# Optimization experiments

Hardware: AMD Instinct MI355X
Metric: run time of the kernel (lower is better)

Reference implementation:

```python
import jax, jax.numpy as jnp
import numpy as np

B, T, V, D, L, FFM = 2, 2048, 50257, 1024, 8, 2


def setup_inputs() -> dict:
    key = jax.random.key(0)
    ks = jax.random.split(key, 10)
    s = 0.02
    return {
        "input_ids": jax.random.randint(ks[0], (B, T), 0, V),
        "embed": jax.random.normal(ks[1], (V, D), jnp.float32) * s,
        "norm1_w": jnp.ones((L, D), jnp.float32),
        "norm2_w": jnp.ones((L, D), jnp.float32),
        "a_diag": jax.random.uniform(ks[2], (L, D), jnp.float32, 0.5, 0.99),
        "W_in": jax.random.normal(ks[3], (L, D, D), jnp.float32) * s,
        "b_in": jnp.zeros((L, D), jnp.float32),
        "W_out": jax.random.normal(ks[4], (L, D, D), jnp.float32) * s,
        "ff_w1": jax.random.normal(ks[5], (L, D, FFM * D), jnp.float32) * s,
        "ff_b1": jnp.zeros((L, FFM * D), jnp.float32),
        "ff_w2": jax.random.normal(ks[6], (L, FFM * D, D), jnp.float32) * s,
        "ff_b2": jnp.zeros((L, D), jnp.float32),
        "final_norm_w": jnp.ones((D,), jnp.float32),
        "lm_head_w": jax.random.normal(ks[7], (V, D), jnp.float32) * s,
    }


def rmsnorm(x, w, eps=1e-6):
    return x * jax.lax.rsqrt(jnp.mean(x * x, axis=-1, keepdims=True) + eps) * w


def chaos_core(x, a, Win, bin_, Wout):
    pre = jnp.einsum('btd,de->bte', x, Win) + bin_  # precompute input drive (parallel)

    def step(s, p):
        s = jnp.tanh(a * s + p)
        return s, s

    s0 = jnp.zeros((x.shape[0], x.shape[-1]), x.dtype)
    _, hs = jax.lax.scan(step, s0, jnp.swapaxes(pre, 0, 1))  # (T, B, D)
    hs = jnp.swapaxes(hs, 0, 1)  # (B, T, D)
    return jnp.einsum('btd,de->bte', hs, Wout)


def reference(input_ids, embed, norm1_w, norm2_w, a_diag, W_in, b_in, W_out,
              ff_w1, ff_b1, ff_w2, ff_b2, final_norm_w, lm_head_w):
    x = embed[input_ids]  # (B, T, D)
    for i in range(L):
        # input_norm -> core -> residual
        x = x + chaos_core(rmsnorm(x, norm1_w[i]), a_diag[i], W_in[i], b_in[i], W_out[i])
        # ff_norm -> FeedForward (Linear -> SiLU -> Linear) -> residual
        h = rmsnorm(x, norm2_w[i])
        h = jax.nn.silu(jnp.einsum('btd,df->btf', h, ff_w1[i]) + ff_b1[i])
        x = x + jnp.einsum('btf,fd->btd', h, ff_w2[i]) + ff_b2[i]
    x = rmsnorm(x, final_norm_w)
    return jnp.einsum('btd,vd->btv', x, lm_head_w)  # logits (B, T, V)
```

## Files before the change

### kernel.cpp

```cpp
#include <hip/hip_runtime.h>

typedef unsigned short u16;
typedef __bf16 bf16x8 __attribute__((ext_vector_type(8)));
typedef float f32x4 __attribute__((ext_vector_type(4)));
typedef unsigned short u16x4 __attribute__((ext_vector_type(4)));

__device__ __forceinline__ u16 f2bf(float f) {
  union { float f; unsigned int u; } v; v.f = f;
  return (u16)((v.u + 0x7FFFu + ((v.u >> 16) & 1u)) >> 16);
}

__device__ __forceinline__ void gload16(const void* g, void* l) {
  __builtin_amdgcn_global_load_lds(
      (const __attribute__((address_space(1))) unsigned int*)g,
      (__attribute__((address_space(3))) unsigned int*)l, 16, 0, 0);
}

__global__ void transpose_cast_kernel(const float* __restrict__ W, u16* __restrict__ WT,
                                      int R, int C) {
  __shared__ float tile[32][33];
  const int tx = threadIdx.x, ty = threadIdx.y;
  const size_t zoff = (size_t)blockIdx.z * R * C;
  const int c0 = blockIdx.x * 32, r0 = blockIdx.y * 32;
#pragma unroll
  for (int k = 0; k < 32; k += 8)
    tile[ty + k][tx] = W[zoff + (size_t)(r0 + ty + k) * C + (c0 + tx)];
  __syncthreads();
#pragma unroll
  for (int k = 0; k < 32; k += 8)
    WT[zoff + (size_t)(c0 + ty + k) * R + (r0 + tx)] = f2bf(tile[tx][ty + k]);
}

__global__ void lm_cast_kernel(const float* __restrict__ lm, u16* __restrict__ out) {
  const int row = blockIdx.x;
  const int t = threadIdx.x;
  u16x4 o = {0, 0, 0, 0};
  if (row < 50257) {
    float4 v = *(const float4*)(lm + (size_t)row * 1024 + t * 4);
    o.x = f2bf(v.x); o.y = f2bf(v.y); o.z = f2bf(v.z); o.w = f2bf(v.w);
  }
  *(u16x4*)(out + (size_t)row * 1024 + t * 4) = o;
}

__global__ void embed_kernel(const int* __restrict__ ids, const float* __restrict__ embed,
                             float* __restrict__ x) {
  const int row = blockIdx.x;
  const int id = ids[row];
  const int t = threadIdx.x;
  *(float4*)(x + (size_t)row * 1024 + t * 4) =
      *(const float4*)(embed + (size_t)id * 1024 + t * 4);
}

__global__ void norm_fused(const float* __restrict__ x, const float* __restrict__ P,
                           const float* __restrict__ bias, const float* __restrict__ w,
                           float* __restrict__ xout, u16* __restrict__ h) {
  const int row = blockIdx.x, tid = threadIdx.x;
  const size_t ro = (size_t)row * 1024 + tid * 4;
  float4 v = *(const float4*)(x + ro);
  if (P) {
    float4 a = *(const float4*)(P + ro);
    float4 b = *(const float4*)(P + 4194304 + ro);
    v.x += a.x + b.x; v.y += a.y + b.y; v.z += a.z + b.z; v.w += a.w + b.w;
  }
  if (bias) {
    float4 bb = *(const float4*)(bias + tid * 4);
    v.x += bb.x; v.y += bb.y; v.z += bb.z; v.w += bb.w;
  }
  if (xout) *(float4*)(xout + ro) = v;
  float ss = v.x * v.x + v.y * v.y + v.z * v.z + v.w * v.w;
#pragma unroll
  for (int off = 32; off; off >>= 1) ss += __shfl_xor(ss, off);
  __shared__ float red[4];
  if ((tid & 63) == 0) red[tid >> 6] = ss;
  __syncthreads();
  const float tot = red[0] + red[1] + red[2] + red[3];
  const float r = rsqrtf(tot * (1.0f / 1024.0f) + 1e-6f);
  float4 wv = *(const float4*)(w + tid * 4);
  u16x4 o;
  o.x = f2bf(v.x * r * wv.x); o.y = f2bf(v.y * r * wv.y);
  o.z = f2bf(v.z * r * wv.z); o.w = f2bf(v.w * r * wv.w);
  *(u16x4*)(h + (size_t)row * 1024 + tid * 4) = o;
}

__device__ __forceinline__ void scan_load(const float* __restrict__ p0,
                                          const float* __restrict__ p1, int tb,
                                          float A2b, float (&buf)[8]) {
#pragma unroll
  for (int j = 0; j < 8; j++)
    buf[j] = fmaf(p0[(size_t)(tb + j) * 1024] + p1[(size_t)(tb + j) * 1024],
                  2.8853900817779268f, A2b);
}

__device__ __forceinline__ void scan_comp(float (&buf)[8], float m2A2, float& r,
                                          u16* __restrict__ o, int tb) {
#pragma unroll
  for (int j = 0; j < 8; j++) {
    float z = fmaf(m2A2, r, buf[j]);
    float e = __builtin_amdgcn_exp2f(z);
    r = __builtin_amdgcn_rcpf(1.0f + e);
    o[(size_t)(tb + j) * 1024] = f2bf(fmaf(-2.0f, r, 1.0f));
  }
}

__global__ __launch_bounds__(256) void scan_kernel(const float* __restrict__ pre,
                                                   const float* __restrict__ a_diag,
                                                   const float* __restrict__ b_in,
                                                   u16* __restrict__ hs) {
  const int T = 2048;
  const int idx = blockIdx.x * 256 + threadIdx.x;
  const int b = idx >> 10, d = idx & 1023;
  const float* p0 = pre + (size_t)b * T * 1024 + d;
  const float* p1 = p0 + 4194304;
  u16* o = hs + (size_t)b * T * 1024 + d;
  const float A2 = a_diag[d] * 2.8853900817779268f;
  const float A2b = fmaf(2.8853900817779268f, b_in[d], A2);
  const float m2A2 = -2.0f * A2;
  float r = 0.5f;
  float b0[8], b1[8], b2[8], b3[8];
  scan_load(p0, p1, 0, A2b, b0); scan_load(p0, p1, 8, A2b, b1);
  scan_load(p0, p1, 16, A2b, b2); scan_load(p0, p1, 24, A2b, b3);
  for (int t0 = 0; t0 < T; t0 += 32) {
    scan_comp(b0, m2A2, r, o, t0);
    if (t0 + 32 < T) scan_load(p0, p1, t0 + 32, A2b, b0);
    scan_comp(b1, m2A2, r, o, t0 + 8);
    if (t0 + 32 < T) scan_load(p0, p1, t0 + 40, A2b, b1);
    scan_comp(b2, m2A2, r, o, t0 + 16);
    if (t0 + 32 < T) scan_load(p0, p1, t0 + 48, A2b, b2);
    scan_comp(b3, m2A2, r, o, t0 + 24);
    if (t0 + 32 < T) scan_load(p0, p1, t0 + 56, A2b, b3);
  }
}

template <int EPI>
__global__ __launch_bounds__(256) void gemm128(
    const u16* __restrict__ A, int lda, const u16* __restrict__ Bw, int ldb,
    const float* __restrict__ bias, float* Cf, u16* __restrict__ Cb, int ldc,
    int Kz, long long Cstride) {
  __shared__ char lds[65536];
  const int tid = threadIdx.x;
  const int lane = tid & 63;
  const int wid = tid >> 6;
  const int wm = wid >> 1, wn = wid & 1;
  const int tm = blockIdx.y * 128, tn = blockIdx.x * 128;
  A += (size_t)blockIdx.z * Kz;
  Bw += (size_t)blockIdx.z * Kz;
  Cf += (size_t)blockIdx.z * Cstride;

  const int srow = tid >> 3;
  const int sxor = ((tid & 7) ^ (srow & 7)) << 4;
  const char* pA = (const char*)A + (size_t)(tm + srow) * lda * 2 + sxor;
  const char* pB = (const char*)Bw + (size_t)(tn + srow) * ldb * 2 + sxor;
  const size_t pstepA = (size_t)32 * lda * 2;
  const size_t pstepB = (size_t)32 * ldb * 2;

#define STG128(kt, bufo)                                             \
  {                                                                  \
    char* d = lds + (bufo) + tid * 16;                               \
    const size_t kb = (size_t)(kt) << 7;                             \
    gload16(pA + kb, d);                                             \
    gload16(pA + pstepA + kb, d + 4096);                             \
    gload16(pA + 2 * pstepA + kb, d + 8192);                         \
    gload16(pA + 3 * pstepA + kb, d + 12288);                        \
    gload16(pB + kb, d + 16384);                                     \
    gload16(pB + pstepB + kb, d + 20480);                            \
    gload16(pB + 2 * pstepB + kb, d + 24576);                        \
    gload16(pB + 3 * pstepB + kb, d + 28672);                        \
  }

  const int lr = lane & 15;
  const int sb0 = (((lane >> 4) ^ (lane & 7)) << 4);
  const int sb[2] = {sb0, sb0 ^ 64};
  const int aB0 = (wm * 64 + lr) * 128;
  const int bB0 = 16384 + (wn * 64 + lr) * 128;

  f32x4 acc[4][4] = {};
  const int nkt = Kz >> 6;

  STG128(0, 0);
  int cur = 0;
  for (int kt = 0; kt < nkt; ++kt) {
    const bool more = (kt + 1 < nkt);
    if (more) STG128(kt + 1, (cur ^ 1) * 32768);
    if (more) { asm volatile("s_waitcnt vmcnt(8)" ::: "memory"); }
    else      { asm volatile("s_waitcnt vmcnt(0)" ::: "memory"); }
    __builtin_amdgcn_s_barrier();
    const char* base = lds + cur * 32768;
    bf16x8 aF[4][2], bF[4][2];
#pragma unroll
    for (int m = 0; m < 4; m++)
#pragma unroll
      for (int ks = 0; ks < 2; ks++) {
        aF[m][ks] = *(const bf16x8*)(base + aB0 + m * 2048 + sb[ks]);
        bF[m][ks] = *(const bf16x8*)(base + bB0 + m * 2048 + sb[ks]);
      }
#pragma unroll
    for (int ks = 0; ks < 2; ks++)
#pragma unroll
      for (int m = 0; m < 4; m++)
#pragma unroll
        for (int n = 0; n < 4; n++)
          acc[m][n] = __builtin_amdgcn_mfma_f32_16x16x32_bf16(aF[m][ks], bF[n][ks],
                                                              acc[m][n], 0, 0, 0);
    __builtin_amdgcn_s_barrier();
    cur ^= 1;
  }
#undef STG128

  const int crow = tm + wm * 64 + ((lane >> 4) << 2);
  const int ccol = tn + wn * 64 + lr;
#pragma unroll
  for (int m = 0; m < 4; m++) {
#pragma unroll
    for (int n = 0; n < 4; n++) {
      const int cg = ccol + n * 16;
      float bb = 0.0f;
      if (EPI == 2) bb = bias[cg];
#pragma unroll
      for (int j = 0; j < 4; j++) {
        const size_t off = (size_t)(crow + m * 16 + j) * ldc + cg;
        const float v = acc[m][n][j] + bb;
        if (EPI == 0) {
          Cf[off] = v;
        } else {
          const float sg = __builtin_amdgcn_rcpf(
              1.0f + __builtin_amdgcn_exp2f(-1.4426950408889634f * v));
          Cb[off] = f2bf(v * sg);
        }
      }
    }
  }
}

__global__ __launch_bounds__(512, 2) void gemm_lm8(
    const u16* __restrict__ A, const u16* __restrict__ Bw,
    float* __restrict__ C, int Nreal) {
  __shared__ char lds[131072];
  const int tid = threadIdx.x;
  const int lane = tid & 63;
  const int wid = tid >> 6;
  const int wr = wid >> 2;
  const int wc = wid & 3;
  const int bid = blockIdx.x;
  const int tm = (((bid & 7) << 1) + ((bid >> 3) & 1)) << 8;
  const int tn = (bid >> 4) << 8;

  const int srow = tid >> 3;
  const int sxor = ((tid & 7) ^ (srow & 7)) << 4;
  const char* pAs = (const char*)A + ((size_t)(tm + srow) << 11) + sxor;
  const char* pBs = (const char*)Bw + ((size_t)(tn + srow) << 11) + sxor;

#define STG(p, h, kt, ro)                                      \
  {                                                            \
    char* d = lds + (ro) + tid * 16;                           \
    const char* s = (p) + ((size_t)(h) << 18) + ((kt) << 7);   \
    gload16(s, d);                                             \
    gload16(s + (64ull << 11), d + 8192);                      \
  }

  const int lr = lane & 15;
  const int sb0 = (((lane >> 4) ^ (lane & 7)) << 4);
  const int sb[2] = {sb0, sb0 ^ 64};
  const int aB = wr * 16384 + lr * 128;
  const int bB = 32768 + (wc >> 1) * 16384 + ((wc & 1) * 64 + lr) * 128;

  bf16x8 aR[4][2], bR[2][2][2];
  f32x4 acc[8][4] = {};

#define LDA_Q(bufo, mq)                                                         \
  _Pragma("unroll") for (int m_ = 0; m_ < 4; m_++)                              \
  _Pragma("unroll") for (int k_ = 0; k_ < 2; k_++)                              \
      aR[m_][k_] = *(const bf16x8*)(lds + (bufo) + aB + (mq)*8192 + m_*2048 + sb[k_]);

#define LDB_Q(bufo, nq)                                                         \
  _Pragma("unroll") for (int n_ = 0; n_ < 2; n_++)                              \
  _Pragma("unroll") for (int k_ = 0; k_ < 2; k_++)                              \
      bR[nq][n_][k_] = *(const bf16x8*)(lds + (bufo) + bB + (nq)*4096 + n_*2048 + sb[k_]);

#define MFMA_Q(mq, nq)                                                          \
  __builtin_amdgcn_s_setprio(1);                                                \
  _Pragma("unroll") for (int m_ = 0; m_ < 4; m_++)                              \
  _Pragma("unroll") for (int n_ = 0; n_ < 2; n_++)                              \
  _Pragma("unroll") for (int k_ = 0; k_ < 2; k_++)                              \
      acc[(mq)*4 + m_][(nq)*2 + n_] = __builtin_amdgcn_mfma_f32_16x16x32_bf16(  \
          aR[m_][k_], bR[nq][n_][k_], acc[(mq)*4 + m_][(nq)*2 + n_], 0, 0, 0);  \
  __builtin_amdgcn_s_setprio(0);

#define BAR() __builtin_amdgcn_s_barrier()
#define LGKM0() asm volatile("s_waitcnt lgkmcnt(0)" ::: "memory")

  STG(pAs, 0, 0, 0);
  STG(pAs, 1, 0, 16384);
  STG(pBs, 0, 0, 32768);
  STG(pBs, 1, 0, 49152);
  STG(pBs, 0, 1, 65536 + 32768);
  STG(pBs, 1, 1, 65536 + 49152);
  asm volatile("s_waitcnt vmcnt(4)" ::: "memory");
  BAR();

  for (int it = 0; it < 8; ++it) {
    const int t1 = 2 * it + 1, t2 = 2 * it + 2, t3 = 2 * it + 3;
    const bool st = (it < 7);
    LDA_Q(0, 0); LDB_Q(0, 0);
    STG(pAs, 0, t1, 65536);
    BAR(); LGKM0(); MFMA_Q(0, 0); BAR();
    LDB_Q(0, 1);
    STG(pAs, 1, t1, 65536 + 16384);
    BAR(); LGKM0(); MFMA_Q(0, 1); BAR();
    LDA_Q(0, 1);
    if (st) STG(pBs, 0, t2, 32768);
    BAR(); LGKM0(); MFMA_Q(1, 0); BAR();
    if (st) STG(pBs, 1, t2, 49152);
    BAR(); LGKM0(); MFMA_Q(1, 1);
    if (st) { asm volatile("s_waitcnt vmcnt(4)" ::: "memory"); }
    else    { asm volatile("s_waitcnt vmcnt(0)" ::: "memory"); }
    BAR();
    LDA_Q(65536, 0); LDB_Q(65536, 0);
    if (st) STG(pAs, 0, t2, 0);
    BAR(); LGKM0(); MFMA_Q(0, 0); BAR();
    LDB_Q(65536, 1);
    if (st) STG(pAs, 1, t2, 16384);
    BAR(); LGKM0(); MFMA_Q(0, 1); BAR();
    LDA_Q(65536, 1);
    if (st) STG(pBs, 0, t3, 65536 + 32768);
    BAR(); LGKM0(); MFMA_Q(1, 0); BAR();
    if (st) STG(pBs, 1, t3, 65536 + 49152);
    BAR(); LGKM0(); MFMA_Q(1, 1);
    if (st) { asm volatile("s_waitcnt vmcnt(4)" ::: "memory"); }
    else    { asm volatile("s_waitcnt vmcnt(0)" ::: "memory"); }
    BAR();
  }
#undef STG
#undef LDA_Q
#undef LDB_Q
#undef MFMA_Q
#undef BAR
#undef LGKM0

  const int crow = tm + wr * 128 + ((lane >> 4) << 2);
  const int ccol = tn + wc * 64 + lr;
#pragma unroll
  for (int M_ = 0; M_ < 8; M_++) {
    const int r = crow + (M_ >> 2) * 64 + (M_ & 3) * 16;
#pragma unroll
    for (int N_ = 0; N_ < 4; N_++) {
      const int cg = ccol + (N_ >> 1) * 32 + (N_ & 1) * 16;
      if (cg < Nreal) {
#pragma unroll
        for (int j = 0; j < 4; j++)
          C[(size_t)(r + j) * Nreal + cg] = acc[M_][N_][j];
      }
    }
  }
}

extern "C" void kernel_launch(void* const* d_in, const int* in_sizes, int n_in,
                              void* d_out, int out_size, void* d_ws, size_t ws_size,
                              hipStream_t stream) {
  const int T = 2048, D = 1024, V = 50257, L = 8;
  const int M = 2 * T;
  const int Vpad = 50432;
  const size_t MD = (size_t)M * D;

  const int* ids = (const int*)d_in[0];
  const float* embed = (const float*)d_in[1];
  const float* norm1_w = (const float*)d_in[2];
  const float* norm2_w = (const float*)d_in[3];
  const float* a_diag = (const float*)d_in[4];
  const float* W_in = (const float*)d_in[5];
  const float* b_in = (const float*)d_in[6];
  const float* W_out = (const float*)d_in[7];
  const float* ff_w1 = (const float*)d_in[8];
  const float* ff_b1 = (const float*)d_in[9];
  const float* ff_w2 = (const float*)d_in[10];
  const float* ff_b2 = (const float*)d_in[11];
  const float* final_norm_w = (const float*)d_in[12];
  const float* lm_head_w = (const float*)d_in[13];

  char* w = (char*)d_ws;
  float* x = (float*)w;    w += MD * 4;
  u16* h = (u16*)w;        w += MD * 2;
  u16* hs = (u16*)w;       w += MD * 2;
  u16* hff = (u16*)w;      w += MD * 2 * 2;
  float* P = (float*)w;    w += MD * 4 * 2;
  float* xP = (float*)w;   w += MD * 4 * 2;
  u16* WinT = (u16*)w;     w += (size_t)L * D * D * 2;
  u16* WoutT = (u16*)w;    w += (size_t)L * D * D * 2;
  u16* ffw1T = (u16*)w;    w += (size_t)L * 2 * D * D * 2;
  u16* ffw2T = (u16*)w;    w += (size_t)L * 2 * D * D * 2;
  u16* lmpad = (u16*)w;    w += (size_t)Vpad * D * 2;

  lm_cast_kernel<<<Vpad, 256, 0, stream>>>(lm_head_w, lmpad);
  transpose_cast_kernel<<<dim3(32, 32, L), dim3(32, 8), 0, stream>>>(W_in, WinT, D, D);
  transpose_cast_kernel<<<dim3(64, 32, L), dim3(32, 8), 0, stream>>>(ff_w1, ffw1T, D, 2 * D);
  transpose_cast_kernel<<<dim3(32, 32, L), dim3(32, 8), 0, stream>>>(W_out, WoutT, D, D);
  transpose_cast_kernel<<<dim3(32, 64, L), dim3(32, 8), 0, stream>>>(ff_w2, ffw2T, 2 * D, D);

  embed_kernel<<<M, 256, 0, stream>>>(ids, embed, x);

  for (int l = 0; l < L; l++) {
    if (l == 0)
      norm_fused<<<M, 256, 0, stream>>>(x, nullptr, nullptr, norm1_w, nullptr, h);
    else
      norm_fused<<<M, 256, 0, stream>>>(x, P, ff_b2 + (size_t)(l - 1) * D,
                                        norm1_w + (size_t)l * D, x, h);
    gemm128<0><<<dim3(8, 32, 2), 256, 0, stream>>>(
        h, D, WinT + (size_t)l * D * D, D, nullptr, P, nullptr, D, 512, (long long)MD);
    scan_kernel<<<8, 256, 0, stream>>>(P, a_diag + (size_t)l * D,
                                       b_in + (size_t)l * D, hs);
    gemm128<0><<<dim3(8, 32, 2), 256, 0, stream>>>(
        hs, D, WoutT + (size_t)l * D * D, D, nullptr, xP, nullptr, D, 512, (long long)MD);
    norm_fused<<<M, 256, 0, stream>>>(x, xP, nullptr, norm2_w + (size_t)l * D, x, h);
    gemm128<2><<<dim3(16, 32, 1), 256, 0, stream>>>(
        h, D, ffw1T + (size_t)l * 2 * D * D, D, ff_b1 + (size_t)l * 2 * D,
        nullptr, hff, 2 * D, 1024, 0);
    gemm128<0><<<dim3(8, 32, 2), 256, 0, stream>>>(
        hff, 2 * D, ffw2T + (size_t)l * 2 * D * D, 2 * D, nullptr, P, nullptr, D,
        1024, (long long)MD);
  }

  norm_fused<<<M, 256, 0, stream>>>(x, P, ff_b2 + (size_t)(L - 1) * D,
                                    final_norm_w, nullptr, h);
  gemm_lm8<<<dim3(8 * 394), 512, 0, stream>>>(h, lmpad, (float*)d_out, V);
}
```

Before: 2.869 ms.

## Replace split-K GEMMs with 64x128 tiles and fuse residual adds into epilogues

Drops the split-K (z=2) 128x128 GEMMs and the partial-sum buffers. It uses a 64x128-tile GEMM over the full K, whose epilogue accumulates straight into the residual x (with bias for FF2). The norm kernels no longer read and sum two partials plus bias, and the scan reads a single pre buffer. The LM head output now uses nontemporal stores. This removes extra partial-buffer traffic and the reduction work, but it gives up K-parallelism and uses read-modify-write epilogues with smaller tiles.

Measured after the change: 3.027 ms. 1.06x slower.

```diff
diff --git a/kernel.cpp b/kernel.cpp
--- a/kernel.cpp
+++ b/kernel.cpp
@@ -51,22 +51,11 @@
       *(const float4*)(embed + (size_t)id * 1024 + t * 4);
 }
 
-__global__ void norm_fused(const float* __restrict__ x, const float* __restrict__ P,
-                           const float* __restrict__ bias, const float* __restrict__ w,
-                           float* __restrict__ xout, u16* __restrict__ h) {
+__global__ void rmsnorm_kernel(const float* __restrict__ x, const float* __restrict__ w,
+                               u16* __restrict__ out) {
   const int row = blockIdx.x, tid = threadIdx.x;
-  const size_t ro = (size_t)row * 1024 + tid * 4;
-  float4 v = *(const float4*)(x + ro);
-  if (P) {
-    float4 a = *(const float4*)(P + ro);
-    float4 b = *(const float4*)(P + 4194304 + ro);
-    v.x += a.x + b.x; v.y += a.y + b.y; v.z += a.z + b.z; v.w += a.w + b.w;
-  }
-  if (bias) {
-    float4 bb = *(const float4*)(bias + tid * 4);
-    v.x += bb.x; v.y += bb.y; v.z += bb.z; v.w += bb.w;
-  }
-  if (xout) *(float4*)(xout + ro) = v;
+  const float* xr = x + (size_t)row * 1024;
+  float4 v = *(const float4*)(xr + tid * 4);
   float ss = v.x * v.x + v.y * v.y + v.z * v.z + v.w * v.w;
 #pragma unroll
   for (int off = 32; off; off >>= 1) ss += __shfl_xor(ss, off);
@@ -79,20 +68,18 @@
   u16x4 o;
   o.x = f2bf(v.x * r * wv.x); o.y = f2bf(v.y * r * wv.y);
   o.z = f2bf(v.z * r * wv.z); o.w = f2bf(v.w * r * wv.w);
-  *(u16x4*)(h + (size_t)row * 1024 + tid * 4) = o;
-}
-
-__device__ __forceinline__ void scan_load(const float* __restrict__ p0,
-                                          const float* __restrict__ p1, int tb,
-                                          float A2b, float (&buf)[8]) {
+  *(u16x4*)(out + (size_t)row * 1024 + tid * 4) = o;
+}
+
+__device__ __forceinline__ void sload(const float* __restrict__ p, int tb,
+                                      float A2b, float (&buf)[8]) {
 #pragma unroll
   for (int j = 0; j < 8; j++)
-    buf[j] = fmaf(p0[(size_t)(tb + j) * 1024] + p1[(size_t)(tb + j) * 1024],
-                  2.8853900817779268f, A2b);
-}
-
-__device__ __forceinline__ void scan_comp(float (&buf)[8], float m2A2, float& r,
-                                          u16* __restrict__ o, int tb) {
+    buf[j] = fmaf(p[(size_t)(tb + j) * 1024], 2.8853900817779268f, A2b);
+}
+
+__device__ __forceinline__ void scomp(float (&buf)[8], float m2A2, float& r,
+                                      u16* __restrict__ o, int tb) {
 #pragma unroll
   for (int j = 0; j < 8; j++) {
     float z = fmaf(m2A2, r, buf[j]);
@@ -109,122 +96,123 @@
   const int T = 2048;
   const int idx = blockIdx.x * 256 + threadIdx.x;
   const int b = idx >> 10, d = idx & 1023;
-  const float* p0 = pre + (size_t)b * T * 1024 + d;
-  const float* p1 = p0 + 4194304;
+  const float* p = pre + (size_t)b * T * 1024 + d;
   u16* o = hs + (size_t)b * T * 1024 + d;
   const float A2 = a_diag[d] * 2.8853900817779268f;
   const float A2b = fmaf(2.8853900817779268f, b_in[d], A2);
   const float m2A2 = -2.0f * A2;
   float r = 0.5f;
   float b0[8], b1[8], b2[8], b3[8];
-  scan_load(p0, p1, 0, A2b, b0); scan_load(p0, p1, 8, A2b, b1);
-  scan_load(p0, p1, 16, A2b, b2); scan_load(p0, p1, 24, A2b, b3);
+  sload(p, 0, A2b, b0); sload(p, 8, A2b, b1);
+  sload(p, 16, A2b, b2); sload(p, 24, A2b, b3);
   for (int t0 = 0; t0 < T; t0 += 32) {
-    scan_comp(b0, m2A2, r, o, t0);
-    if (t0 + 32 < T) scan_load(p0, p1, t0 + 32, A2b, b0);
-    scan_comp(b1, m2A2, r, o, t0 + 8);
-    if (t0 + 32 < T) scan_load(p0, p1, t0 + 40, A2b, b1);
-    scan_comp(b2, m2A2, r, o, t0 + 16);
-    if (t0 + 32 < T) scan_load(p0, p1, t0 + 48, A2b, b2);
-    scan_comp(b3, m2A2, r, o, t0 + 24);
-    if (t0 + 32 < T) scan_load(p0, p1, t0 + 56, A2b, b3);
+    scomp(b0, m2A2, r, o, t0);
+    if (t0 + 32 < T) sload(p, t0 + 32, A2b, b0);
+    scomp(b1, m2A2, r, o, t0 + 8);
+    if (t0 + 32 < T) sload(p, t0 + 40, A2b, b1);
+    scomp(b2, m2A2, r, o, t0 + 16);
+    if (t0 + 32 < T) sload(p, t0 + 48, A2b, b2);
+    scomp(b3, m2A2, r, o, t0 + 24);
+    if (t0 + 32 < T) sload(p, t0 + 56, A2b, b3);
   }
 }
 
 template <int EPI>
-__global__ __launch_bounds__(256) void gemm128(
+__global__ __launch_bounds__(256) void gemmL(
     const u16* __restrict__ A, int lda, const u16* __restrict__ Bw, int ldb,
-    const float* __restrict__ bias, float* Cf, u16* __restrict__ Cb, int ldc,
-    int Kz, long long Cstride) {
-  __shared__ char lds[65536];
+    const float* __restrict__ bias, float* Cf, u16* __restrict__ Cb,
+    int ldc, int K) {
+  __shared__ char lds[49152];
   const int tid = threadIdx.x;
   const int lane = tid & 63;
-  const int wid = tid >> 6;
-  const int wm = wid >> 1, wn = wid & 1;
-  const int tm = blockIdx.y * 128, tn = blockIdx.x * 128;
-  A += (size_t)blockIdx.z * Kz;
-  Bw += (size_t)blockIdx.z * Kz;
-  Cf += (size_t)blockIdx.z * Cstride;
+  const int wc = tid >> 6;
+  const int tm = blockIdx.y * 64, tn = blockIdx.x * 128;
+  const int lr = lane & 15;
+  const int sb0 = ((lane >> 4) ^ (lane & 7)) << 4;
 
   const int srow = tid >> 3;
-  const int sxor = ((tid & 7) ^ (srow & 7)) << 4;
-  const char* pA = (const char*)A + (size_t)(tm + srow) * lda * 2 + sxor;
-  const char* pB = (const char*)Bw + (size_t)(tn + srow) * ldb * 2 + sxor;
-  const size_t pstepA = (size_t)32 * lda * 2;
-  const size_t pstepB = (size_t)32 * ldb * 2;
-
-#define STG128(kt, bufo)                                             \
-  {                                                                  \
-    char* d = lds + (bufo) + tid * 16;                               \
-    const size_t kb = (size_t)(kt) << 7;                             \
-    gload16(pA + kb, d);                                             \
-    gload16(pA + pstepA + kb, d + 4096);                             \
-    gload16(pA + 2 * pstepA + kb, d + 8192);                         \
-    gload16(pA + 3 * pstepA + kb, d + 12288);                        \
-    gload16(pB + kb, d + 16384);                                     \
-    gload16(pB + pstepB + kb, d + 20480);                            \
-    gload16(pB + 2 * pstepB + kb, d + 24576);                        \
-    gload16(pB + 3 * pstepB + kb, d + 28672);                        \
-  }
-
-  const int lr = lane & 15;
-  const int sb0 = (((lane >> 4) ^ (lane & 7)) << 4);
-  const int sb[2] = {sb0, sb0 ^ 64};
-  const int aB0 = (wm * 64 + lr) * 128;
-  const int bB0 = 16384 + (wn * 64 + lr) * 128;
-
-  f32x4 acc[4][4] = {};
-  const int nkt = Kz >> 6;
-
-  STG128(0, 0);
+  const int sxs = ((tid & 7) ^ (srow & 7)) << 4;
+  const char* pA = (const char*)A + (size_t)(tm + srow) * lda * 2 + sxs;
+  const char* pB = (const char*)Bw + (size_t)(tn + srow) * ldb * 2 + sxs;
+  const size_t a32 = (size_t)lda * 64;
+  const size_t b32 = (size_t)ldb * 64;
+
+#define STGL(kt, bufo)                                \
+  {                                                   \
+    char* d = lds + (bufo) + tid * 16;                \
+    const size_t kb = (size_t)(kt) << 7;              \
+    gload16(pA + kb, d);                              \
+    gload16(pA + a32 + kb, d + 4096);                 \
+    gload16(pB + kb, d + 8192);                       \
+    gload16(pB + b32 + kb, d + 12288);                \
+    gload16(pB + 2 * b32 + kb, d + 16384);            \
+    gload16(pB + 3 * b32 + kb, d + 20480);            \
+  }
+
+  f32x4 acc[4][2] = {};
+  const int nkt = K >> 6;
+
+  STGL(0, 0);
   int cur = 0;
   for (int kt = 0; kt < nkt; ++kt) {
-    const bool more = (kt + 1 < nkt);
-    if (more) STG128(kt + 1, (cur ^ 1) * 32768);
-    if (more) { asm volatile("s_waitcnt vmcnt(8)" ::: "memory"); }
-    else      { asm volatile("s_waitcnt vmcnt(0)" ::: "memory"); }
+    if (kt + 1 < nkt) {
+      STGL(kt + 1, (cur ^ 1) * 24576);
+      asm volatile("s_waitcnt vmcnt(6)" ::: "memory");
+    } else {
+      asm volatile("s_waitcnt vmcnt(0)" ::: "memory");
+    }
     __builtin_amdgcn_s_barrier();
-    const char* base = lds + cur * 32768;
-    bf16x8 aF[4][2], bF[4][2];
+    const char* base = lds + cur * 24576;
+    bf16x8 aF[4][2], bF[2][2];
 #pragma unroll
     for (int m = 0; m < 4; m++)
 #pragma unroll
-      for (int ks = 0; ks < 2; ks++) {
-        aF[m][ks] = *(const bf16x8*)(base + aB0 + m * 2048 + sb[ks]);
-        bF[m][ks] = *(const bf16x8*)(base + bB0 + m * 2048 + sb[ks]);
-      }
+      for (int ks = 0; ks < 2; ks++)
+        aF[m][ks] =
+            *(const bf16x8*)(base + (m * 16 + lr) * 128 + (sb0 ^ (ks << 6)));
+#pragma unroll
+    for (int n = 0; n < 2; n++)
+#pragma unroll
+      for (int ks = 0; ks < 2; ks++)
+        bF[n][ks] = *(const bf16x8*)(base + 8192 +
+                                     (wc * 32 + n * 16 + lr) * 128 +
+                                     (sb0 ^ (ks << 6)));
 #pragma unroll
     for (int ks = 0; ks < 2; ks++)
 #pragma unroll
       for (int m = 0; m < 4; m++)
 #pragma unroll
-        for (int n = 0; n < 4; n++)
-          acc[m][n] = __builtin_amdgcn_mfma_f32_16x16x32_bf16(aF[m][ks], bF[n][ks],
-                                                              acc[m][n], 0, 0, 0);
+        for (int n = 0; n < 2; n++)
+          acc[m][n] = __builtin_amdgcn_mfma_f32_16x16x32_bf16(
+              aF[m][ks], bF[n][ks], acc[m][n], 0, 0, 0);
     __builtin_amdgcn_s_barrier();
     cur ^= 1;
   }
-#undef STG128
-
-  const int crow = tm + wm * 64 + ((lane >> 4) << 2);
-  const int ccol = tn + wn * 64 + lr;
+#undef STGL
+
+  const int crow = tm + ((lane >> 4) << 2);
+  const int ccol = tn + wc * 32 + lr;
 #pragma unroll
   for (int m = 0; m < 4; m++) {
 #pragma unroll
-    for (int n = 0; n < 4; n++) {
+    for (int n = 0; n < 2; n++) {
       const int cg = ccol + n * 16;
       float bb = 0.0f;
-      if (EPI == 2) bb = bias[cg];
+      if (EPI == 2 || EPI == 3) bb = bias[cg];
 #pragma unroll
       for (int j = 0; j < 4; j++) {
         const size_t off = (size_t)(crow + m * 16 + j) * ldc + cg;
         const float v = acc[m][n][j] + bb;
         if (EPI == 0) {
           Cf[off] = v;
-        } else {
+        } else if (EPI == 1) {
+          Cf[off] += v;
+        } else if (EPI == 2) {
           const float sg = __builtin_amdgcn_rcpf(
               1.0f + __builtin_amdgcn_exp2f(-1.4426950408889634f * v));
           Cb[off] = f2bf(v * sg);
+        } else {
+          Cf[off] += v;
         }
       }
     }
@@ -347,7 +335,8 @@
       if (cg < Nreal) {
 #pragma unroll
         for (int j = 0; j < 4; j++)
-          C[(size_t)(r + j) * Nreal + cg] = acc[M_][N_][j];
+          __builtin_nontemporal_store(acc[M_][N_][j],
+                                      &C[(size_t)(r + j) * Nreal + cg]);
       }
     }
   }
@@ -356,13 +345,13 @@
 extern "C" void kernel_launch(void* const* d_in, const int* in_sizes, int n_in,
                               void* d_out, int out_size, void* d_ws, size_t ws_size,
                               hipStream_t stream) {
-  const int T = 2048, D = 1024, V = 50257, L = 8;
-  const int M = 2 * T;
+  const int D = 1024, V = 50257, L = 8;
+  const int M = 4096;
   const int Vpad = 50432;
   const size_t MD = (size_t)M * D;
 
   const int* ids = (const int*)d_in[0];
-  const float* embed = (const float*)d_in[1];
+  const float* embedw = (const float*)d_in[1];
   const float* norm1_w = (const float*)d_in[2];
   const float* norm2_w = (const float*)d_in[3];
   const float* a_diag = (const float*)d_in[4];
@@ -377,17 +366,16 @@
   const float* lm_head_w = (const float*)d_in[13];
 
   char* w = (char*)d_ws;
-  float* x = (float*)w;    w += MD * 4;
-  u16* h = (u16*)w;        w += MD * 2;
-  u16* hs = (u16*)w;       w += MD * 2;
-  u16* hff = (u16*)w;      w += MD * 2 * 2;
-  float* P = (float*)w;    w += MD * 4 * 2;
-  float* xP = (float*)w;   w += MD * 4 * 2;
-  u16* WinT = (u16*)w;     w += (size_t)L * D * D * 2;
-  u16* WoutT = (u16*)w;    w += (size_t)L * D * D * 2;
-  u16* ffw1T = (u16*)w;    w += (size_t)L * 2 * D * D * 2;
-  u16* ffw2T = (u16*)w;    w += (size_t)L * 2 * D * D * 2;
-  u16* lmpad = (u16*)w;    w += (size_t)Vpad * D * 2;
+  float* x = (float*)w;   w += MD * 4;
+  u16* h = (u16*)w;       w += MD * 2;
+  float* pre = (float*)w; w += MD * 4;
+  u16* hs = (u16*)w;      w += MD * 2;
+  u16* hff = (u16*)w;     w += MD * 2 * 2;
+  u16* WinT = (u16*)w;    w += (size_t)L * D * D * 2;
+  u16* WoutT = (u16*)w;   w += (size_t)L * D * D * 2;
+  u16* ffw1T = (u16*)w;   w += (size_t)L * 2 * D * D * 2;
+  u16* ffw2T = (u16*)w;   w += (size_t)L * 2 * D * D * 2;
+  u16* lmpad = (u16*)w;   w += (size_t)Vpad * D * 2;
 
   lm_cast_kernel<<<Vpad, 256, 0, stream>>>(lm_head_w, lmpad);
   transpose_cast_kernel<<<dim3(32, 32, L), dim3(32, 8), 0, stream>>>(W_in, WinT, D, D);
@@ -395,30 +383,25 @@
   transpose_cast_kernel<<<dim3(32, 32, L), dim3(32, 8), 0, stream>>>(W_out, WoutT, D, D);
   transpose_cast_kernel<<<dim3(32, 64, L), dim3(32, 8), 0, stream>>>(ff_w2, ffw2T, 2 * D, D);
 
-  embed_kernel<<<M, 256, 0, stream>>>(ids, embed, x);
+  embed_kernel<<<M, 256, 0, stream>>>(ids, embedw, x);
 
   for (int l = 0; l < L; l++) {
-    if (l == 0)
-      norm_fused<<<M, 256, 0, stream>>>(x, nullptr, nullptr, norm1_w, nullptr, h);
-    else
-      norm_fused<<<M, 256, 0, stream>>>(x, P, ff_b2 + (size_t)(l - 1) * D,
-                                        norm1_w + (size_t)l * D, x, h);
-    gemm128<0><<<dim3(8, 32, 2), 256, 0, stream>>>(
-        h, D, WinT + (size_t)l * D * D, D, nullptr, P, nullptr, D, 512, (long long)MD);
-    scan_kernel<<<8, 256, 0, stream>>>(P, a_diag + (size_t)l * D,
+    rmsnorm_kernel<<<M, 256, 0, stream>>>(x, norm1_w + (size_t)l * D, h);
+    gemmL<0><<<dim3(8, 64), 256, 0, stream>>>(
+        h, D, WinT + (size_t)l * D * D, D, nullptr, pre, nullptr, D, D);
+    scan_kernel<<<8, 256, 0, stream>>>(pre, a_diag + (size_t)l * D,
                                        b_in + (size_t)l * D, hs);
-    gemm128<0><<<dim3(8, 32, 2), 256, 0, stream>>>(
-        hs, D, WoutT + (size_t)l * D * D, D, nullptr, xP, nullptr, D, 512, (long long)MD);
-    norm_fused<<<M, 256, 0, stream>>>(x, xP, nullptr, norm2_w + (size_t)l * D, x, h);
-    gemm128<2><<<dim3(16, 32, 1), 256, 0, stream>>>(
+    gemmL<1><<<dim3(8, 64), 256, 0, stream>>>(
+        hs, D, WoutT + (size_t)l * D * D, D, nullptr, x, nullptr, D, D);
+    rmsnorm_kernel<<<M, 256, 0, stream>>>(x, norm2_w + (size_t)l * D, h);
+    gemmL<2><<<dim3(16, 64), 256, 0, stream>>>(
         h, D, ffw1T + (size_t)l * 2 * D * D, D, ff_b1 + (size_t)l * 2 * D,
-        nullptr, hff, 2 * D, 1024, 0);
-    gemm128<0><<<dim3(8, 32, 2), 256, 0, stream>>>(
-        hff, 2 * D, ffw2T + (size_t)l * 2 * D * D, 2 * D, nullptr, P, nullptr, D,
-        1024, (long long)MD);
-  }
-
-  norm_fused<<<M, 256, 0, stream>>>(x, P, ff_b2 + (size_t)(L - 1) * D,
-                                    final_norm_w, nullptr, h);
+        nullptr, hff, 2 * D, D);
+    gemmL<3><<<dim3(8, 64), 256, 0, stream>>>(
+        hff, 2 * D, ffw2T + (size_t)l * 2 * D * D, 2 * D,
+        ff_b2 + (size_t)l * D, x, nullptr, D, 2 * D);
+  }
+
+  rmsnorm_kernel<<<M, 256, 0, stream>>>(x, final_norm_w, h);
   gemm_lm8<<<dim3(8 * 394), 512, 0, stream>>>(h, lmpad, (float*)d_out, V);
 }
```
